# Optimization experiments

Hardware: AMD Instinct MI355X
Metric: run time of the kernel (lower is better)

Reference implementation:

```python
import jax, jax.numpy as jnp
import numpy as np

N, D, S, R = 50000, 256, 6, 4
EPS = 1e-5

def group_norm1(x, w, b):
    # GroupNorm with 1 group on [N, C]: normalize each row over channels
    m = jnp.mean(x, axis=-1, keepdims=True)
    v = jnp.mean(jnp.square(x - m), axis=-1, keepdims=True)
    return (x - m) * jax.lax.rsqrt(v + EPS) * w + b

def setup_inputs() -> dict:
    key = jax.random.key(0)
    ks = jax.random.split(key, 10)
    scale = 1.0 / np.sqrt(D)
    return {
        'lane_features': jax.random.normal(ks[0], (N, D), jnp.float32),
        'W_ctr': jax.random.normal(ks[1], (R, D, D), jnp.float32) * scale,
        'norm_w': jnp.ones((R, D), jnp.float32),
        'norm_b': jnp.zeros((R, D), jnp.float32),
        'W_ctr2': jax.random.normal(ks[2], (R, D, D), jnp.float32) * scale,
        'ctr2_norm_w': jnp.ones((R, D), jnp.float32),
        'ctr2_norm_b': jnp.zeros((R, D), jnp.float32),
        'W_pre': jax.random.normal(ks[3], (R, S, D, D), jnp.float32) * scale,
        'W_suc': jax.random.normal(ks[4], (R, S, D, D), jnp.float32) * scale,
        'pre_idx': jax.random.randint(ks[5], (S, N), 0, N, jnp.int32),
        'suc_idx': jax.random.randint(ks[6], (S, N), 0, N, jnp.int32),
        'n_hop_pre': jax.random.randint(ks[7], (S, N), 0, N, jnp.int32),
        'n_hop_suc': jax.random.randint(ks[8], (S, N), 0, N, jnp.int32),
    }

def reference(lane_features, W_ctr, norm_w, norm_b, W_ctr2, ctr2_norm_w,
              ctr2_norm_b, W_pre, W_suc, pre_idx, suc_idx, n_hop_pre, n_hop_suc):
    x = lane_features
    res = x
    for i in range(R):
        # ctr linear (bias=False): x @ W.T
        temp = x @ W_ctr[i].T
        for k in range(S):
            # pre branch: gather n_hop_pre, linear, scatter-add at suc
            msg_pre = x[n_hop_pre[k]] @ W_pre[i, k].T
            temp = temp.at[suc_idx[k]].add(msg_pre)
            # suc branch: gather n_hop_suc, linear, scatter-add at pre
            msg_suc = x[n_hop_suc[k]] @ W_suc[i, k].T
            temp = temp.at[pre_idx[k]].add(msg_suc)
        x = jax.nn.relu(group_norm1(temp, norm_w[i], norm_b[i]))
        # ctr2: Linear(no bias) + GroupNorm, no activation
        x = group_norm1(x @ W_ctr2[i].T, ctr2_norm_w[i], ctr2_norm_b[i])
        x = jax.nn.relu(x + res)
        res = x
    return x
```

## Files before the change

### kernel.cpp

```cpp
#include <hip/hip_runtime.h>

#define NROWS 50000
#define DIM   256
#define SHOPS 6
#define ROUNDS 4
#define EPSV  1e-5f
#define ND ((size_t)NROWS * DIM)
#define NB  196
#define EMAXR 36864
#define EMAXND ((size_t)EMAXR * DIM)

typedef _Float16 f16x8 __attribute__((ext_vector_type(8)));
typedef _Float16 f16x4 __attribute__((ext_vector_type(4)));
typedef float    f32x4 __attribute__((ext_vector_type(4)));

#define GLDS16(GP, LP) \
    __builtin_amdgcn_global_load_lds((const __attribute__((address_space(1))) unsigned*)(GP), \
                                     (__attribute__((address_space(3))) unsigned*)(LP), 16, 0, 0)

__device__ __forceinline__ int imin(int a, int b) { return a < b ? a : b; }

__global__ __launch_bounds__(256)
void gemm_p(const _Float16* __restrict__ A, const _Float16* __restrict__ WH,
            int s0, int s1, int nz, _Float16* __restrict__ C0,
            _Float16* __restrict__ CZ, int ctr0, int nwg,
            const int* __restrict__ LIVE, const int* __restrict__ Ecnt,
            int sbase)
{
    __shared__ _Float16 lds[3][8192];
    char* ldsb = (char*)lds;

    const int bid = blockIdx.x;
    const int q   = nwg >> 3, r = nwg & 7;
    const int xcd = bid & 7,  ii = bid >> 3;
    const int g   = (xcd < r) ? xcd * (q + 1) + ii
                              : r * (q + 1) + (xcd - r) * q + ii;
    const int j   = g / (2 * nz);
    const int sub = g - j * 2 * nz;
    const int by  = sub & 1;
    const size_t z = sub >> 1;
    int xp, jj;
    if (j < 7 * 49) { xp = j / 49; jj = j % 49; }
    else            { xp = 7; jj = j - 7 * 49; }
    const int bx = jj * 8 + xp;

    const int seg = sbase + (int)z;
    const int En  = (seg >= 0) ? Ecnt[seg] : NROWS;
    const int bm0 = bx * 128;
    if (bm0 >= En) return;
    const int* lvp = (seg >= 0) ? LIVE + (size_t)seg * NROWS : nullptr;

    const int tid = threadIdx.x;
    const int l   = tid & 63;
    const int w   = tid >> 6;
    const int wm  = w & 1;
    const int wn  = w >> 1;
    const int bn0 = by * 128;
    const int lr  = l & 15;
    const int sl  = l >> 4;

    const int wslot = (z == 0) ? s0 : s1 + (int)z;
    const char* Ab = (const char*)A;
    const char* Wb = (const char*)(WH + (size_t)wslot * (DIM * DIM));

    int arow[2], slog[2], wrow[2];
    #pragma unroll
    for (int qq = 0; qq < 2; ++qq) {
        const int c   = (w * 2 + qq) * 64 + l;
        const int row = c >> 2;
        slog[qq] = (c & 3) ^ ((row >> 1) & 3);
        const int cl = imin(bm0 + row, En - 1);
        arow[qq] = lvp ? lvp[cl] : cl;
        wrow[qq] = bn0 + row;
    }

    f32x4 acc[4][4];
    #pragma unroll
    for (int mt = 0; mt < 4; ++mt)
        #pragma unroll
        for (int nt = 0; nt < 4; ++nt)
            acc[mt][nt] = (f32x4){0.f, 0.f, 0.f, 0.f};

    auto stage = [&](int step, int buf) {
        const int kt64 = step * 64;
        char* base = ldsb + buf * 16384;
        #pragma unroll
        for (int qq = 0; qq < 2; ++qq) {
            GLDS16(Ab + (size_t)arow[qq] * 512 + kt64 + slog[qq] * 16,
                   base + (w * 2 + qq) * 1024);
            GLDS16(Wb + (size_t)wrow[qq] * 512 + kt64 + slog[qq] * 16,
                   base + 8192 + (w * 2 + qq) * 1024);
        }
    };

    auto compute = [&](int buf) {
        const char* base = ldsb + buf * 16384;
        f16x8 af[4], bf[4];
        #pragma unroll
        for (int mt = 0; mt < 4; ++mt) {
            const int row = wm * 64 + mt * 16 + lr;
            af[mt] = *(const f16x8*)(base + row * 64 + ((sl ^ ((row >> 1) & 3)) << 4));
        }
        #pragma unroll
        for (int nt = 0; nt < 4; ++nt) {
            const int row = wn * 64 + nt * 16 + lr;
            bf[nt] = *(const f16x8*)(base + 8192 + row * 64 + ((sl ^ ((row >> 1) & 3)) << 4));
        }
        #pragma unroll
        for (int mt = 0; mt < 4; ++mt)
            #pragma unroll
            for (int nt = 0; nt < 4; ++nt)
                acc[mt][nt] = __builtin_amdgcn_mfma_f32_16x16x32_f16(
                    af[mt], bf[nt], acc[mt][nt], 0, 0, 0);
    };

    stage(0, 0);
    stage(1, 1);
    #pragma unroll
    for (int t = 0; t < 7; ++t) {
        asm volatile("s_waitcnt vmcnt(4)" ::: "memory");
        __builtin_amdgcn_s_barrier();
        __builtin_amdgcn_sched_barrier(0);
        if (t < 6) stage(t + 2, (t + 2) % 3);
        compute(t % 3);
    }
    asm volatile("s_waitcnt vmcnt(0)" ::: "memory");
    __builtin_amdgcn_s_barrier();
    __builtin_amdgcn_sched_barrier(0);
    compute(7 % 3);

    __syncthreads();
    _Float16* et = (_Float16*)ldsb;
    #pragma unroll
    for (int mt = 0; mt < 4; ++mt)
        #pragma unroll
        for (int nt = 0; nt < 4; ++nt)
            #pragma unroll
            for (int jv = 0; jv < 4; ++jv) {
                const int row = wm * 64 + mt * 16 + sl * 4 + jv;
                const int col = wn * 64 + nt * 16 + lr;
                et[row * 136 + col] = (_Float16)acc[mt][nt][jv];
            }
    __syncthreads();
    _Float16* Cb = (ctr0 && z == 0) ? C0 : CZ + (size_t)((int)z - ctr0) * EMAXND;
    #pragma unroll
    for (int qq = 0; qq < 8; ++qq) {
        const int c   = qq * 256 + tid;
        const int row = c >> 4;
        const int cc  = (c & 15) * 8;
        const int orow = bm0 + row;
        if (orow < En) {
            const f16x8 v = *(const f16x8*)(et + row * 136 + cc);
            *(f16x8*)(Cb + (size_t)orow * DIM + bn0 + cc) = v;
        }
    }
}

__global__ __launch_bounds__(512)
void gemm_gn(const _Float16* __restrict__ A, const _Float16* __restrict__ WH,
             int wslot, const float* __restrict__ gw, const float* __restrict__ gb,
             float* __restrict__ X, _Float16* __restrict__ Xh, int writex)
{
    __shared__ char ldsb[49152 + 4096];
    float* sArr  = (float*)(ldsb + 49152);
    float* ssArr = sArr + 512;

    const int tid = threadIdx.x;
    const int l   = tid & 63;
    const int w   = tid >> 6;
    const int wm  = w & 1;
    const int wn  = w >> 1;
    const int bm0 = blockIdx.x * 128;
    const int lr  = l & 15;
    const int sl  = l >> 4;

    const char* Ab = (const char*)A;
    const char* Wb = (const char*)(WH + (size_t)wslot * (DIM * DIM));

    int arow, aslog, wr0, ws0, wr1, ws1;
    {
        int c = tid, row = c >> 2;
        aslog = (c & 3) ^ ((row >> 1) & 3);
        arow  = imin(bm0 + row, NROWS - 1);
        ws0 = aslog; wr0 = row;
        c = tid + 512; row = c >> 2;
        ws1 = (c & 3) ^ ((row >> 1) & 3); wr1 = row;
    }

    f32x4 acc[4][4];
    #pragma unroll
    for (int mt = 0; mt < 4; ++mt)
        #pragma unroll
        for (int nt = 0; nt < 4; ++nt)
            acc[mt][nt] = (f32x4){0.f, 0.f, 0.f, 0.f};

    auto stage = [&](int step, int buf) {
        const int kt64 = step * 64;
        char* base = ldsb + buf * 24576;
        GLDS16(Ab + (size_t)arow * 512 + kt64 + aslog * 16, base + w * 1024);
        GLDS16(Wb + (size_t)wr0 * 512 + kt64 + ws0 * 16, base + 8192 + w * 1024);
        GLDS16(Wb + (size_t)wr1 * 512 + kt64 + ws1 * 16, base + 16384 + w * 1024);
    };

    auto compute = [&](int buf) {
        const char* base = ldsb + buf * 24576;
        f16x8 af[4], bf[4];
        #pragma unroll
        for (int mt = 0; mt < 4; ++mt) {
            const int row = wm * 64 + mt * 16 + lr;
            af[mt] = *(const f16x8*)(base + row * 64 + ((sl ^ ((row >> 1) & 3)) << 4));
        }
        #pragma unroll
        for (int nt = 0; nt < 4; ++nt) {
            const int row = wn * 64 + nt * 16 + lr;
            bf[nt] = *(const f16x8*)(base + 8192 + row * 64 + ((sl ^ ((row >> 1) & 3)) << 4));
        }
        #pragma unroll
        for (int mt = 0; mt < 4; ++mt)
            #pragma unroll
            for (int nt = 0; nt < 4; ++nt)
                acc[mt][nt] = __builtin_amdgcn_mfma_f32_16x16x32_f16(
                    af[mt], bf[nt], acc[mt][nt], 0, 0, 0);
    };

    stage(0, 0);
    #pragma unroll
    for (int t = 0; t < 8; ++t) {
        asm volatile("s_waitcnt vmcnt(0)" ::: "memory");
        __builtin_amdgcn_s_barrier();
        __builtin_amdgcn_sched_barrier(0);
        if (t < 7) stage(t + 1, (t + 1) & 1);
        compute(t & 1);
    }

    float sp[4][4], ssp[4][4];
    #pragma unroll
    for (int mt = 0; mt < 4; ++mt)
        #pragma unroll
        for (int jv = 0; jv < 4; ++jv) {
            float s = 0.f, ss = 0.f;
            #pragma unroll
            for (int nt = 0; nt < 4; ++nt) {
                const float v = acc[mt][nt][jv];
                s += v; ss += v * v;
            }
            sp[mt][jv] = s; ssp[mt][jv] = ss;
        }
    #pragma unroll
    for (int off = 1; off < 16; off <<= 1)
        #pragma unroll
        for (int mt = 0; mt < 4; ++mt)
            #pragma unroll
            for (int jv = 0; jv < 4; ++jv) {
                sp[mt][jv]  += __shfl_xor(sp[mt][jv], off);
                ssp[mt][jv] += __shfl_xor(ssp[mt][jv], off);
            }
    __syncthreads();
    if (lr == 0) {
        #pragma unroll
        for (int mt = 0; mt < 4; ++mt)
            #pragma unroll
            for (int jv = 0; jv < 4; ++jv) {
                const int row = wm * 64 + mt * 16 + sl * 4 + jv;
                sArr[wn * 128 + row]  = sp[mt][jv];
                ssArr[wn * 128 + row] = ssp[mt][jv];
            }
    }
    __syncthreads();
    float mv[4][4], iv[4][4];
    #pragma unroll
    for (int mt = 0; mt < 4; ++mt)
        #pragma unroll
        for (int jv = 0; jv < 4; ++jv) {
            const int row = wm * 64 + mt * 16 + sl * 4 + jv;
            const float S  = sArr[row] + sArr[128 + row] + sArr[256 + row] + sArr[384 + row];
            const float SS = ssArr[row] + ssArr[128 + row] + ssArr[256 + row] + ssArr[384 + row];
            const float m  = S * (1.0f / DIM);
            mv[mt][jv] = m;
            iv[mt][jv] = rsqrtf(SS * (1.0f / DIM) - m * m + EPSV);
        }
    float gwv[4], gbv[4];
    #pragma unroll
    for (int nt = 0; nt < 4; ++nt) {
        const int col = wn * 64 + nt * 16 + lr;
        gwv[nt] = gw[col]; gbv[nt] = gb[col];
    }

    _Float16* et = (_Float16*)ldsb;
    #pragma unroll
    for (int half = 0; half < 2; ++half) {
        __syncthreads();
        if (wm == half) {
            #pragma unroll
            for (int mt = 0; mt < 4; ++mt)
                #pragma unroll
                for (int nt = 0; nt < 4; ++nt)
                    #pragma unroll
                    for (int jv = 0; jv < 4; ++jv) {
                        const int rl  = mt * 16 + sl * 4 + jv;
                        const int col = wn * 64 + nt * 16 + lr;
                        et[rl * 264 + col] = (_Float16)((acc[mt][nt][jv] - mv[mt][jv])
                                                        * iv[mt][jv] * gwv[nt] + gbv[nt]);
                    }
        }
        __syncthreads();
        #pragma unroll
        for (int qq = 0; qq < 4; ++qq) {
            const int c   = qq * 512 + tid;
            const int row = c >> 5;
            const int cc  = (c & 31) * 8;
            const int orow = bm0 + half * 64 + row;
            if (orow < NROWS) {
                const f16x8 y = *(const f16x8*)(et + row * 264 + cc);
                const f16x8 rr = *(const f16x8*)(Xh + (size_t)orow * DIM + cc);
                float o[8];
                #pragma unroll
                for (int e = 0; e < 8; ++e)
                    o[e] = fmaxf((float)y[e] + (float)rr[e], 0.f);
                f16x8 oh;
                #pragma unroll
                for (int e = 0; e < 8; ++e) oh[e] = (_Float16)o[e];
                *(f16x8*)(Xh + (size_t)orow * DIM + cc) = oh;
                if (writex) {
                    float* xp = X + (size_t)orow * DIM + cc;
                    *(float4*)xp       = make_float4(o[0], o[1], o[2], o[3]);
                    *(float4*)(xp + 4) = make_float4(o[4], o[5], o[6], o[7]);
                }
            }
        }
    }
}

__global__ __launch_bounds__(256)
void convert_w(const float* __restrict__ Wctr, const float* __restrict__ Wctr2,
               const float* __restrict__ Wpre, const float* __restrict__ Wsuc,
               _Float16* __restrict__ WH)
{
    const size_t i4 = (size_t)blockIdx.x * 256 + threadIdx.x;
    const size_t NT = (size_t)56 * DIM * DIM / 4;
    if (i4 >= NT) return;
    const size_t e = i4 * 4;
    const int slot = (int)(e >> 16);
    const int off  = (int)(e & 65535);
    const float* src;
    if (slot < 48) {
        const int r = slot / 12, s = slot % 12, k = s >> 1, dir = s & 1;
        src = (dir ? Wsuc : Wpre) + (((size_t)r * SHOPS + k) << 16) + off;
    } else if (slot < 52) {
        src = Wctr + ((size_t)(slot - 48) << 16) + off;
    } else {
        src = Wctr2 + ((size_t)(slot - 52) << 16) + off;
    }
    const float4 v = *(const float4*)src;
    f16x4 h;
    h[0] = (_Float16)v.x; h[1] = (_Float16)v.y;
    h[2] = (_Float16)v.z; h[3] = (_Float16)v.w;
    *(f16x4*)(WH + e) = h;
}

__global__ __launch_bounds__(256)
void init_x(const float* __restrict__ lane, _Float16* __restrict__ Xh)
{
    const size_t i4 = (size_t)blockIdx.x * 256 + threadIdx.x;
    if (i4 >= ND / 4) return;
    const float4 v = *(const float4*)(lane + i4 * 4);
    f16x4 h;
    h[0] = (_Float16)v.x; h[1] = (_Float16)v.y;
    h[2] = (_Float16)v.z; h[3] = (_Float16)v.w;
    *(f16x4*)(Xh + i4 * 4) = h;
}

__global__ __launch_bounds__(256)
void markk(const int* __restrict__ nhp, const int* __restrict__ nhs,
           int* __restrict__ mark)
{
    const int i = blockIdx.x * 256 + threadIdx.x;
    if (i >= NROWS) return;
    const int s = blockIdx.y;
    const int k = s >> 1, dir = s & 1;
    const int* gp = (dir ? nhs : nhp) + k * NROWS;
    mark[(size_t)s * NROWS + gp[i]] = 1;
}

__global__ __launch_bounds__(256)
void mscan1(const int* __restrict__ mark, int* __restrict__ mrank,
            int* __restrict__ msum)
{
    __shared__ int wsum[4];
    const int s = blockIdx.y;
    const int tid = threadIdx.x, lane = tid & 63, wv = tid >> 6;
    const int i = blockIdx.x * 256 + tid;
    const int c = (i < NROWS) ? mark[(size_t)s * NROWS + i] : 0;
    int v = c;
    #pragma unroll
    for (int off = 1; off < 64; off <<= 1) {
        const int t = __shfl_up(v, off);
        if (lane >= off) v += t;
    }
    if (lane == 63) wsum[wv] = v;
    __syncthreads();
    int add = 0;
    for (int w = 0; w < wv; ++w) add += wsum[w];
    if (i < NROWS) mrank[(size_t)s * NROWS + i] = add + v - c;
    if (tid == 255) msum[s * 256 + blockIdx.x] = wsum[0] + wsum[1] + wsum[2] + wsum[3];
}

__global__ __launch_bounds__(256)
void mscan2(const int* __restrict__ msum, int* __restrict__ mbpre,
            int* __restrict__ Ecnt)
{
    __shared__ int wsum[4];
    const int s = blockIdx.x;
    const int tid = threadIdx.x, lane = tid & 63, wv = tid >> 6;
    const int c = (tid < NB) ? msum[s * 256 + tid] : 0;
    int v = c;
    #pragma unroll
    for (int off = 1; off < 64; off <<= 1) {
        const int t = __shfl_up(v, off);
        if (lane >= off) v += t;
    }
    if (lane == 63) wsum[wv] = v;
    __syncthreads();
    int add = 0;
    for (int w = 0; w < wv; ++w) add += wsum[w];
    if (tid < NB) mbpre[s * 256 + tid] = add + v - c;
    if (tid == 0) Ecnt[s] = wsum[0] + wsum[1] + wsum[2] + wsum[3];
}

__global__ __launch_bounds__(256)
void mscan3(const int* __restrict__ mark, int* __restrict__ mrank,
            const int* __restrict__ mbpre, int* __restrict__ live)
{
    const int i = blockIdx.x * 256 + threadIdx.x;
    if (i >= NROWS) return;
    const int s = blockIdx.y;
    const size_t o = (size_t)s * NROWS + i;
    const int rk = mrank[o] + mbpre[s * 256 + blockIdx.x];
    mrank[o] = rk;
    if (mark[o]) live[(size_t)s * NROWS + rk] = i;
}

__global__ __launch_bounds__(256)
void count_kernel(const int* __restrict__ pidx, const int* __restrict__ sidx,
                  int* __restrict__ counts, int* __restrict__ countsA)
{
    const int i = blockIdx.x * 256 + threadIdx.x;
    if (i >= NROWS) return;
    const int s = blockIdx.y;
    const int k = s >> 1, dir = s & 1;
    const int* scp = (dir ? pidx : sidx) + k * NROWS;
    const int dst = scp[i];
    atomicAdd(&counts[dst], 1);
    if (s < 6) atomicAdd(&countsA[dst], 1);
}

__global__ __launch_bounds__(256)
void scan1_kernel(const int* __restrict__ counts, int* __restrict__ offs,
                  int* __restrict__ bsum)
{
    __shared__ int wsum[4];
    const int tid = threadIdx.x, lane = tid & 63, wv = tid >> 6;
    const int i = blockIdx.x * 256 + tid;
    const int c = (i < NROWS) ? counts[i] : 0;
    int v = c;
    #pragma unroll
    for (int off = 1; off < 64; off <<= 1) {
        const int t = __shfl_up(v, off);
        if (lane >= off) v += t;
    }
    if (lane == 63) wsum[wv] = v;
    __syncthreads();
    int add = 0;
    for (int w = 0; w < wv; ++w) add += wsum[w];
    if (i < NROWS) offs[i] = add + v - c;
    if (tid == 255) bsum[blockIdx.x] = wsum[0] + wsum[1] + wsum[2] + wsum[3];
}

__global__ __launch_bounds__(256)
void scan2_kernel(const int* __restrict__ bsum, int* __restrict__ bpre)
{
    __shared__ int wsum[4];
    const int tid = threadIdx.x, lane = tid & 63, wv = tid >> 6;
    const int c = (tid < NB) ? bsum[tid] : 0;
    int v = c;
    #pragma unroll
    for (int off = 1; off < 64; off <<= 1) {
        const int t = __shfl_up(v, off);
        if (lane >= off) v += t;
    }
    if (lane == 63) wsum[wv] = v;
    __syncthreads();
    int add = 0;
    for (int w = 0; w < wv; ++w) add += wsum[w];
    if (tid < NB) bpre[tid] = add + v - c;
}

__global__ __launch_bounds__(256)
void scan3_kernel(int* __restrict__ offs, const int* __restrict__ bpre,
                  const int* __restrict__ countsA,
                  int* __restrict__ cursorA, int* __restrict__ cursorB,
                  int* __restrict__ mid)
{
    const int i = blockIdx.x * 256 + threadIdx.x;
    if (i < NROWS) {
        const int v = offs[i] + bpre[blockIdx.x];
        offs[i] = v;
        cursorA[i] = v;
        const int m = v + countsA[i];
        mid[i] = m;
        cursorB[i] = m;
    }
    if (i == 0) offs[NROWS] = 12 * NROWS;
}

__global__ __launch_bounds__(256)
void fill_kernel(const int* __restrict__ pidx, const int* __restrict__ sidx,
                 const int* __restrict__ nhp, const int* __restrict__ nhs,
                 const int* __restrict__ mrank,
                 int* __restrict__ cursorA, int* __restrict__ cursorB,
                 int* __restrict__ entries)
{
    const int i = blockIdx.x * 256 + threadIdx.x;
    if (i >= NROWS) return;
    const int s = blockIdx.y;
    const int k = s >> 1, dir = s & 1;
    const int* scp = (dir ? pidx : sidx) + k * NROWS;
    const int* gp  = (dir ? nhs  : nhp)  + k * NROWS;
    const int dst = scp[i];
    const int pos = (s < 6) ? atomicAdd(&cursorA[dst], 1)
                            : atomicAdd(&cursorB[dst], 1);
    entries[pos] = (s << 16) | mrank[(size_t)s * NROWS + gp[i]];
}

template<int FIRST, int LAST>
__global__ __launch_bounds__(256)
void combine_f16(const _Float16* __restrict__ YC, _Float16* __restrict__ TEMP16,
                 const _Float16* __restrict__ YB,
                 const int* __restrict__ offsets, const int* __restrict__ mid,
                 const int* __restrict__ entries,
                 int c0, int nch, int half,
                 const float* __restrict__ gw, const float* __restrict__ gb,
                 _Float16* __restrict__ Hh)
{
    const int lane = threadIdx.x & 63;
    const int wv   = threadIdx.x >> 6;
    const int r    = blockIdx.x * 4 + wv;
    if (r >= NROWS) return;
    const size_t rowoff = (size_t)r * DIM + lane * 4;

    const f16x4 ivv = FIRST ? *(const f16x4*)(YC + rowoff)
                            : *(const f16x4*)(TEMP16 + rowoff);
    float4 acc;
    acc.x = (float)ivv[0]; acc.y = (float)ivv[1];
    acc.z = (float)ivv[2]; acc.w = (float)ivv[3];

    int e0, e1;
    if (half == 0)      { e0 = offsets[r]; e1 = mid[r]; }
    else if (half == 1) { e0 = mid[r];     e1 = offsets[r + 1]; }
    else                { e0 = offsets[r]; e1 = offsets[r + 1]; }

    for (int e = e0; e < e1; ++e) {
        const int ent = entries[e];
        const int s = ent >> 16;
        if ((unsigned)(s - c0) < (unsigned)nch) {
            const f16x4 yv = *(const f16x4*)(YB + (size_t)(s - c0) * EMAXND
                                             + (size_t)(ent & 0xFFFF) * DIM + lane * 4);
            acc.x += (float)yv[0]; acc.y += (float)yv[1];
            acc.z += (float)yv[2]; acc.w += (float)yv[3];
        }
    }

    if (LAST) {
        float s  = acc.x + acc.y + acc.z + acc.w;
        float ss = acc.x * acc.x + acc.y * acc.y + acc.z * acc.z + acc.w * acc.w;
        #pragma unroll
        for (int off = 32; off >= 1; off >>= 1) {
            s  += __shfl_xor(s, off);
            ss += __shfl_xor(ss, off);
        }
        const float m   = s * (1.0f / DIM);
        const float var = ss * (1.0f / DIM) - m * m;
        const float inv = rsqrtf(var + EPSV);
        const float4 wv4 = *(const float4*)(gw + lane * 4);
        const float4 bv4 = *(const float4*)(gb + lane * 4);
        f16x4 o;
        o[0] = (_Float16)fmaxf((acc.x - m) * inv * wv4.x + bv4.x, 0.f);
        o[1] = (_Float16)fmaxf((acc.y - m) * inv * wv4.y + bv4.y, 0.f);
        o[2] = (_Float16)fmaxf((acc.z - m) * inv * wv4.z + bv4.z, 0.f);
        o[3] = (_Float16)fmaxf((acc.w - m) * inv * wv4.w + bv4.w, 0.f);
        *(f16x4*)(Hh + rowoff) = o;
    } else {
        f16x4 o;
        o[0] = (_Float16)acc.x; o[1] = (_Float16)acc.y;
        o[2] = (_Float16)acc.z; o[3] = (_Float16)acc.w;
        *(f16x4*)(TEMP16 + rowoff) = o;
    }
}

extern "C" void kernel_launch(void* const* d_in, const int* in_sizes, int n_in,
                              void* d_out, int out_size, void* d_ws, size_t ws_size,
                              hipStream_t stream)
{
    const float* lane   = (const float*)d_in[0];
    const float* W_ctr  = (const float*)d_in[1];
    const float* norm_w = (const float*)d_in[2];
    const float* norm_b = (const float*)d_in[3];
    const float* W_ctr2 = (const float*)d_in[4];
    const float* c2w    = (const float*)d_in[5];
    const float* c2b    = (const float*)d_in[6];
    const float* W_pre  = (const float*)d_in[7];
    const float* W_suc  = (const float*)d_in[8];
    const int*   pidx   = (const int*)d_in[9];
    const int*   sidx   = (const int*)d_in[10];
    const int*   nhp    = (const int*)d_in[11];
    const int*   nhs    = (const int*)d_in[12];

    float* X = (float*)d_out;

    char* p = (char*)d_ws;
    int* counts  = (int*)p; p += (size_t)NROWS * 4;
    int* countsA = (int*)p; p += (size_t)NROWS * 4;
    int* offsets = (int*)p; p += (size_t)(NROWS + 4) * 4;
    int* mid     = (int*)p; p += (size_t)NROWS * 4;
    int* cursorA = (int*)p; p += (size_t)NROWS * 4;
    int* cursorB = (int*)p; p += (size_t)NROWS * 4;
    int* bsum    = (int*)p; p += 256 * 4;
    int* bpre    = (int*)p; p += 256 * 4;
    int* msum    = (int*)p; p += 12 * 256 * 4;
    int* mbpre   = (int*)p; p += 12 * 256 * 4;
    int* Ecnt    = (int*)p; p += 16 * 4;
    int* entries = (int*)p; p += (size_t)12 * NROWS * 4;
    int* LIVE    = (int*)p; p += (size_t)12 * NROWS * 4;
    p = (char*)(((uintptr_t)p + 15) & ~(uintptr_t)15);
    _Float16* Xh   = (_Float16*)p; p += ND * 2;
    _Float16* Hh   = (_Float16*)p; p += ND * 2;
    _Float16* T16  = (_Float16*)p; p += ND * 2;
    _Float16* WH   = (_Float16*)p; p += (size_t)56 * DIM * DIM * 2;
    p = (char*)(((uintptr_t)p + 15) & ~(uintptr_t)15);
    _Float16* YC   = (_Float16*)p; p += ND * 2;
    _Float16* YBUF = (_Float16*)p;

    int* mark  = (int*)YBUF;
    int* mrank = mark + (size_t)12 * NROWS;

    const size_t used = (size_t)(p - (char*)d_ws);
    const size_t slotb = EMAXND * 2;
    int nslot = (ws_size > used) ? (int)((ws_size - used) / slotb) : 1;
    if (nslot < 1) nslot = 1;
    int CH;
    if (nslot >= 12) CH = 12;
    else {
        CH = nslot;
        const int nchunks = (12 + CH - 1) / CH;
        CH = (12 + nchunks - 1) / nchunks;
    }

    const dim3 blk(256);
    const int  gnBlocks = (NROWS + 3) / 4;
    const int  cwBlocks = (int)(((size_t)56 * DIM * DIM / 4 + 255) / 256);
    const int  ixBlocks = (int)((ND / 4 + 255) / 256);

    convert_w<<<cwBlocks, blk, 0, stream>>>(W_ctr, W_ctr2, W_pre, W_suc, WH);
    init_x<<<ixBlocks, blk, 0, stream>>>(lane, Xh);
    hipMemsetAsync(counts, 0, NROWS * sizeof(int), stream);
    hipMemsetAsync(countsA, 0, NROWS * sizeof(int), stream);
    hipMemsetAsync(mark, 0, (size_t)12 * NROWS * sizeof(int), stream);
    markk<<<dim3(NB, 12), blk, 0, stream>>>(nhp, nhs, mark);
    mscan1<<<dim3(NB, 12), blk, 0, stream>>>(mark, mrank, msum);
    mscan2<<<12, blk, 0, stream>>>(msum, mbpre, Ecnt);
    mscan3<<<dim3(NB, 12), blk, 0, stream>>>(mark, mrank, mbpre, LIVE);
    count_kernel<<<dim3(NB, 12), blk, 0, stream>>>(pidx, sidx, counts, countsA);
    scan1_kernel<<<NB, blk, 0, stream>>>(counts, offsets, bsum);
    scan2_kernel<<<1, blk, 0, stream>>>(bsum, bpre);
    scan3_kernel<<<NB, blk, 0, stream>>>(offsets, bpre, countsA,
                                         cursorA, cursorB, mid);
    fill_kernel<<<dim3(NB, 12), blk, 0, stream>>>(pidx, sidx, nhp, nhs, mrank,
                                                  cursorA, cursorB, entries);

    for (int i = 0; i < ROUNDS; ++i) {
        for (int c0 = 0; c0 < 12; c0 += CH) {
            const int nz = (12 - c0 < CH) ? (12 - c0) : CH;
            const bool first = (c0 == 0);
            const bool last  = (c0 + nz >= 12);
            const int ctr0  = first ? 1 : 0;
            const int slots = nz + ctr0;
            const int nwg   = 391 * 2 * slots;
            gemm_p<<<dim3(nwg), blk, 0, stream>>>(
                Xh, WH, first ? (48 + i) : (i * 12 + c0), i * 12 + c0 - ctr0,
                slots, YC, YBUF, ctr0, nwg, LIVE, Ecnt, c0 - ctr0);
            const int half = (CH == 6) ? (first ? 0 : 1) : -1;
            if (first && last)
                combine_f16<1, 1><<<gnBlocks, blk, 0, stream>>>(YC, T16, YBUF,
                    offsets, mid, entries, c0, nz, half,
                    norm_w + i * DIM, norm_b + i * DIM, Hh);
            else if (first)
                combine_f16<1, 0><<<gnBlocks, blk, 0, stream>>>(YC, T16, YBUF,
                    offsets, mid, entries, c0, nz, half,
                    norm_w + i * DIM, norm_b + i * DIM, Hh);
            else if (last)
                combine_f16<0, 1><<<gnBlocks, blk, 0, stream>>>(YC, T16, YBUF,
                    offsets, mid, entries, c0, nz, half,
                    norm_w + i * DIM, norm_b + i * DIM, Hh);
            else
                combine_f16<0, 0><<<gnBlocks, blk, 0, stream>>>(YC, T16, YBUF,
                    offsets, mid, entries, c0, nz, half,
                    norm_w + i * DIM, norm_b + i * DIM, Hh);
        }
        gemm_gn<<<391, 512, 0, stream>>>(Hh, WH, 52 + i, c2w + i * DIM,
                                         c2b + i * DIM, X, Xh,
                                         (i == ROUNDS - 1) ? 1 : 0);
    }
}
```

Before: 1.077 ms.

## Triple-buffer gemm_gn, fuse setup kernels, prefetch combine gathers, shrink buffers

gemm_gn moves from double to triple buffering, with a partial vmcnt wait so two stages stay in flight. The setup kernels are merged: weight and input conversion run in one launch, and the mark, count and scan passes run in three launches over 13 grid rows, cutting launch overhead. combine_f16 now prefetches up to 20 gathered rows into registers before accumulating, to expose memory-level parallelism. The workspace is reorganised: YC reuses the output buffer, T16 aliases Hh when 12 slots fit, and EMAXR is lowered. The lower EMAXR risks overflow if a slot's live count exceeds 32768, and the chunk-range filter in combine is removed.

After: 950.3 us, median of 2. 1.13x faster.

```diff
diff --git a/kernel.cpp b/kernel.cpp
--- a/kernel.cpp
+++ b/kernel.cpp
@@ -7,7 +7,7 @@
 #define EPSV  1e-5f
 #define ND ((size_t)NROWS * DIM)
 #define NB  196
-#define EMAXR 36864
+#define EMAXR 32768
 #define EMAXND ((size_t)EMAXR * DIM)
 
 typedef _Float16 f16x8 __attribute__((ext_vector_type(8)));
@@ -161,8 +161,8 @@
              int wslot, const float* __restrict__ gw, const float* __restrict__ gb,
              float* __restrict__ X, _Float16* __restrict__ Xh, int writex)
 {
-    __shared__ char ldsb[49152 + 4096];
-    float* sArr  = (float*)(ldsb + 49152);
+    __shared__ char ldsb[3 * 24576 + 4096];
+    float* sArr  = (float*)(ldsb + 73728);
     float* ssArr = sArr + 512;
 
     const int tid = threadIdx.x;
@@ -224,14 +224,19 @@
     };
 
     stage(0, 0);
-    #pragma unroll
-    for (int t = 0; t < 8; ++t) {
-        asm volatile("s_waitcnt vmcnt(0)" ::: "memory");
+    stage(1, 1);
+    #pragma unroll
+    for (int t = 0; t < 7; ++t) {
+        asm volatile("s_waitcnt vmcnt(3)" ::: "memory");
         __builtin_amdgcn_s_barrier();
         __builtin_amdgcn_sched_barrier(0);
-        if (t < 7) stage(t + 1, (t + 1) & 1);
-        compute(t & 1);
-    }
+        if (t < 6) stage(t + 2, (t + 2) % 3);
+        compute(t % 3);
+    }
+    asm volatile("s_waitcnt vmcnt(0)" ::: "memory");
+    __builtin_amdgcn_s_barrier();
+    __builtin_amdgcn_sched_barrier(0);
+    compute(7 % 3);
 
     float sp[4][4], ssp[4][4];
     #pragma unroll
@@ -332,65 +337,72 @@
 }
 
 __global__ __launch_bounds__(256)
-void convert_w(const float* __restrict__ Wctr, const float* __restrict__ Wctr2,
-               const float* __restrict__ Wpre, const float* __restrict__ Wsuc,
-               _Float16* __restrict__ WH)
-{
-    const size_t i4 = (size_t)blockIdx.x * 256 + threadIdx.x;
-    const size_t NT = (size_t)56 * DIM * DIM / 4;
-    if (i4 >= NT) return;
-    const size_t e = i4 * 4;
-    const int slot = (int)(e >> 16);
-    const int off  = (int)(e & 65535);
-    const float* src;
-    if (slot < 48) {
-        const int r = slot / 12, s = slot % 12, k = s >> 1, dir = s & 1;
-        src = (dir ? Wsuc : Wpre) + (((size_t)r * SHOPS + k) << 16) + off;
-    } else if (slot < 52) {
-        src = Wctr + ((size_t)(slot - 48) << 16) + off;
+void cvt_init(const float* __restrict__ lane, _Float16* __restrict__ Xh,
+              const float* __restrict__ Wctr, const float* __restrict__ Wctr2,
+              const float* __restrict__ Wpre, const float* __restrict__ Wsuc,
+              _Float16* __restrict__ WH)
+{
+    const int bid = blockIdx.x;
+    if (bid < 12500) {
+        const size_t i4 = (size_t)bid * 256 + threadIdx.x;
+        if (i4 >= ND / 4) return;
+        const float4 v = *(const float4*)(lane + i4 * 4);
+        f16x4 h;
+        h[0] = (_Float16)v.x; h[1] = (_Float16)v.y;
+        h[2] = (_Float16)v.z; h[3] = (_Float16)v.w;
+        *(f16x4*)(Xh + i4 * 4) = h;
     } else {
-        src = Wctr2 + ((size_t)(slot - 52) << 16) + off;
-    }
-    const float4 v = *(const float4*)src;
-    f16x4 h;
-    h[0] = (_Float16)v.x; h[1] = (_Float16)v.y;
-    h[2] = (_Float16)v.z; h[3] = (_Float16)v.w;
-    *(f16x4*)(WH + e) = h;
-}
-
-__global__ __launch_bounds__(256)
-void init_x(const float* __restrict__ lane, _Float16* __restrict__ Xh)
-{
-    const size_t i4 = (size_t)blockIdx.x * 256 + threadIdx.x;
-    if (i4 >= ND / 4) return;
-    const float4 v = *(const float4*)(lane + i4 * 4);
-    f16x4 h;
-    h[0] = (_Float16)v.x; h[1] = (_Float16)v.y;
-    h[2] = (_Float16)v.z; h[3] = (_Float16)v.w;
-    *(f16x4*)(Xh + i4 * 4) = h;
-}
-
-__global__ __launch_bounds__(256)
-void markk(const int* __restrict__ nhp, const int* __restrict__ nhs,
-           int* __restrict__ mark)
+        const size_t i4 = (size_t)(bid - 12500) * 256 + threadIdx.x;
+        const size_t NT = (size_t)56 * DIM * DIM / 4;
+        if (i4 >= NT) return;
+        const size_t e = i4 * 4;
+        const int slot = (int)(e >> 16);
+        const int off  = (int)(e & 65535);
+        const float* src;
+        if (slot < 48) {
+            const int r = slot / 12, s = slot % 12, k = s >> 1, dir = s & 1;
+            src = (dir ? Wsuc : Wpre) + (((size_t)r * SHOPS + k) << 16) + off;
+        } else if (slot < 52) {
+            src = Wctr + ((size_t)(slot - 48) << 16) + off;
+        } else {
+            src = Wctr2 + ((size_t)(slot - 52) << 16) + off;
+        }
+        const float4 v = *(const float4*)src;
+        f16x4 h;
+        h[0] = (_Float16)v.x; h[1] = (_Float16)v.y;
+        h[2] = (_Float16)v.z; h[3] = (_Float16)v.w;
+        *(f16x4*)(WH + e) = h;
+    }
+}
+
+__global__ __launch_bounds__(256)
+void markcount(const int* __restrict__ pidx, const int* __restrict__ sidx,
+               const int* __restrict__ nhp, const int* __restrict__ nhs,
+               int* __restrict__ mark, int* __restrict__ counts,
+               int* __restrict__ countsA)
 {
     const int i = blockIdx.x * 256 + threadIdx.x;
     if (i >= NROWS) return;
     const int s = blockIdx.y;
     const int k = s >> 1, dir = s & 1;
-    const int* gp = (dir ? nhs : nhp) + k * NROWS;
+    const int* gp  = (dir ? nhs  : nhp)  + k * NROWS;
+    const int* scp = (dir ? pidx : sidx) + k * NROWS;
     mark[(size_t)s * NROWS + gp[i]] = 1;
-}
-
-__global__ __launch_bounds__(256)
-void mscan1(const int* __restrict__ mark, int* __restrict__ mrank,
-            int* __restrict__ msum)
+    const int dst = scp[i];
+    atomicAdd(&counts[dst], 1);
+    if (s < 6) atomicAdd(&countsA[dst], 1);
+}
+
+__global__ __launch_bounds__(256)
+void pscan1(const int* __restrict__ mark, const int* __restrict__ counts,
+            int* __restrict__ mrank, int* __restrict__ msum,
+            int* __restrict__ offs, int* __restrict__ bsum)
 {
     __shared__ int wsum[4];
-    const int s = blockIdx.y;
+    const int y = blockIdx.y;
     const int tid = threadIdx.x, lane = tid & 63, wv = tid >> 6;
     const int i = blockIdx.x * 256 + tid;
-    const int c = (i < NROWS) ? mark[(size_t)s * NROWS + i] : 0;
+    const int c = (i < NROWS) ? ((y < 12) ? mark[(size_t)y * NROWS + i] : counts[i]) : 0;
     int v = c;
     #pragma unroll
     for (int off = 1; off < 64; off <<= 1) {
@@ -401,18 +413,27 @@
     __syncthreads();
     int add = 0;
     for (int w = 0; w < wv; ++w) add += wsum[w];
-    if (i < NROWS) mrank[(size_t)s * NROWS + i] = add + v - c;
-    if (tid == 255) msum[s * 256 + blockIdx.x] = wsum[0] + wsum[1] + wsum[2] + wsum[3];
-}
-
-__global__ __launch_bounds__(256)
-void mscan2(const int* __restrict__ msum, int* __restrict__ mbpre,
+    const int excl = add + v - c;
+    if (i < NROWS) {
+        if (y < 12) mrank[(size_t)y * NROWS + i] = excl;
+        else        offs[i] = excl;
+    }
+    if (tid == 255) {
+        const int tot = wsum[0] + wsum[1] + wsum[2] + wsum[3];
+        if (y < 12) msum[y * 256 + blockIdx.x] = tot;
+        else        bsum[blockIdx.x] = tot;
+    }
+}
+
+__global__ __launch_bounds__(256)
+void pscan2(const int* __restrict__ msum, const int* __restrict__ bsum,
+            int* __restrict__ mbpre, int* __restrict__ bpre,
             int* __restrict__ Ecnt)
 {
     __shared__ int wsum[4];
-    const int s = blockIdx.x;
+    const int y = blockIdx.x;
     const int tid = threadIdx.x, lane = tid & 63, wv = tid >> 6;
-    const int c = (tid < NB) ? msum[s * 256 + tid] : 0;
+    const int c = (tid < NB) ? ((y < 12) ? msum[y * 256 + tid] : bsum[tid]) : 0;
     int v = c;
     #pragma unroll
     for (int off = 1; off < 64; off <<= 1) {
@@ -423,94 +444,40 @@
     __syncthreads();
     int add = 0;
     for (int w = 0; w < wv; ++w) add += wsum[w];
-    if (tid < NB) mbpre[s * 256 + tid] = add + v - c;
-    if (tid == 0) Ecnt[s] = wsum[0] + wsum[1] + wsum[2] + wsum[3];
-}
-
-__global__ __launch_bounds__(256)
-void mscan3(const int* __restrict__ mark, int* __restrict__ mrank,
-            const int* __restrict__ mbpre, int* __restrict__ live)
+    if (tid < NB) {
+        if (y < 12) mbpre[y * 256 + tid] = add + v - c;
+        else        bpre[tid] = add + v - c;
+    }
+    if (tid == 0 && y < 12)
+        Ecnt[y] = wsum[0] + wsum[1] + wsum[2] + wsum[3];
+}
+
+__global__ __launch_bounds__(256)
+void pscan3(const int* __restrict__ mark, int* __restrict__ mrank,
+            const int* __restrict__ mbpre, int* __restrict__ live,
+            int* __restrict__ offs, const int* __restrict__ bpre,
+            const int* __restrict__ countsA, int* __restrict__ cursorA,
+            int* __restrict__ cursorB, int* __restrict__ mid)
 {
     const int i = blockIdx.x * 256 + threadIdx.x;
-    if (i >= NROWS) return;
-    const int s = blockIdx.y;
-    const size_t o = (size_t)s * NROWS + i;
-    const int rk = mrank[o] + mbpre[s * 256 + blockIdx.x];
-    mrank[o] = rk;
-    if (mark[o]) live[(size_t)s * NROWS + rk] = i;
-}
-
-__global__ __launch_bounds__(256)
-void count_kernel(const int* __restrict__ pidx, const int* __restrict__ sidx,
-                  int* __restrict__ counts, int* __restrict__ countsA)
-{
-    const int i = blockIdx.x * 256 + threadIdx.x;
-    if (i >= NROWS) return;
-    const int s = blockIdx.y;
-    const int k = s >> 1, dir = s & 1;
-    const int* scp = (dir ? pidx : sidx) + k * NROWS;
-    const int dst = scp[i];
-    atomicAdd(&counts[dst], 1);
-    if (s < 6) atomicAdd(&countsA[dst], 1);
-}
-
-__global__ __launch_bounds__(256)
-void scan1_kernel(const int* __restrict__ counts, int* __restrict__ offs,
-                  int* __restrict__ bsum)
-{
-    __shared__ int wsum[4];
-    const int tid = threadIdx.x, lane = tid & 63, wv = tid >> 6;
-    const int i = blockIdx.x * 256 + tid;
-    const int c = (i < NROWS) ? counts[i] : 0;
-    int v = c;
-    #pragma unroll
-    for (int off = 1; off < 64; off <<= 1) {
-        const int t = __shfl_up(v, off);
-        if (lane >= off) v += t;
-    }
-    if (lane == 63) wsum[wv] = v;
-    __syncthreads();
-    int add = 0;
-    for (int w = 0; w < wv; ++w) add += wsum[w];
-    if (i < NROWS) offs[i] = add + v - c;
-    if (tid == 255) bsum[blockIdx.x] = wsum[0] + wsum[1] + wsum[2] + wsum[3];
-}
-
-__global__ __launch_bounds__(256)
-void scan2_kernel(const int* __restrict__ bsum, int* __restrict__ bpre)
-{
-    __shared__ int wsum[4];
-    const int tid = threadIdx.x, lane = tid & 63, wv = tid >> 6;
-    const int c = (tid < NB) ? bsum[tid] : 0;
-    int v = c;
-    #pragma unroll
-    for (int off = 1; off < 64; off <<= 1) {
-        const int t = __shfl_up(v, off);
-        if (lane >= off) v += t;
-    }
-    if (lane == 63) wsum[wv] = v;
-    __syncthreads();
-    int add = 0;
-    for (int w = 0; w < wv; ++w) add += wsum[w];
-    if (tid < NB) bpre[tid] = add + v - c;
-}
-
-__global__ __launch_bounds__(256)
-void scan3_kernel(int* __restrict__ offs, const int* __restrict__ bpre,
-                  const int* __restrict__ countsA,
-                  int* __restrict__ cursorA, int* __restrict__ cursorB,
-                  int* __restrict__ mid)
-{
-    const int i = blockIdx.x * 256 + threadIdx.x;
-    if (i < NROWS) {
-        const int v = offs[i] + bpre[blockIdx.x];
-        offs[i] = v;
-        cursorA[i] = v;
-        const int m = v + countsA[i];
-        mid[i] = m;
-        cursorB[i] = m;
-    }
-    if (i == 0) offs[NROWS] = 12 * NROWS;
+    const int y = blockIdx.y;
+    if (y < 12) {
+        if (i >= NROWS) return;
+        const size_t o = (size_t)y * NROWS + i;
+        const int rk = mrank[o] + mbpre[y * 256 + blockIdx.x];
+        mrank[o] = rk;
+        if (mark[o]) live[(size_t)y * NROWS + rk] = i;
+    } else {
+        if (i < NROWS) {
+            const int v = offs[i] + bpre[blockIdx.x];
+            offs[i] = v;
+            cursorA[i] = v;
+            const int m = v + countsA[i];
+            mid[i] = m;
+            cursorB[i] = m;
+        }
+        if (i == 0) offs[NROWS] = 12 * NROWS;
+    }
 }
 
 __global__ __launch_bounds__(256)
@@ -532,13 +499,14 @@
     entries[pos] = (s << 16) | mrank[(size_t)s * NROWS + gp[i]];
 }
 
+#define PF 20
 template<int FIRST, int LAST>
 __global__ __launch_bounds__(256)
 void combine_f16(const _Float16* __restrict__ YC, _Float16* __restrict__ TEMP16,
                  const _Float16* __restrict__ YB,
                  const int* __restrict__ offsets, const int* __restrict__ mid,
                  const int* __restrict__ entries,
-                 int c0, int nch, int half,
+                 int c0, int half,
                  const float* __restrict__ gw, const float* __restrict__ gb,
                  _Float16* __restrict__ Hh)
 {
@@ -559,15 +527,30 @@
     else if (half == 1) { e0 = mid[r];     e1 = offsets[r + 1]; }
     else                { e0 = offsets[r]; e1 = offsets[r + 1]; }
 
-    for (int e = e0; e < e1; ++e) {
+    const int n  = e1 - e0;
+    const int nf = n < PF ? n : PF;
+    f16x4 buf[PF];
+    #pragma unroll
+    for (int t = 0; t < PF; ++t) {
+        if (t < nf) {
+            const int ent = entries[e0 + t];
+            buf[t] = *(const f16x4*)(YB + (size_t)((ent >> 16) - c0) * EMAXND
+                                     + (size_t)(ent & 0xFFFF) * DIM + lane * 4);
+        }
+    }
+    #pragma unroll
+    for (int t = 0; t < PF; ++t) {
+        if (t < nf) {
+            acc.x += (float)buf[t][0]; acc.y += (float)buf[t][1];
+            acc.z += (float)buf[t][2]; acc.w += (float)buf[t][3];
+        }
+    }
+    for (int e = e0 + nf; e < e1; ++e) {
         const int ent = entries[e];
-        const int s = ent >> 16;
-        if ((unsigned)(s - c0) < (unsigned)nch) {
-            const f16x4 yv = *(const f16x4*)(YB + (size_t)(s - c0) * EMAXND
-                                             + (size_t)(ent & 0xFFFF) * DIM + lane * 4);
-            acc.x += (float)yv[0]; acc.y += (float)yv[1];
-            acc.z += (float)yv[2]; acc.w += (float)yv[3];
-        }
+        const f16x4 yv = *(const f16x4*)(YB + (size_t)((ent >> 16) - c0) * EMAXND
+                                         + (size_t)(ent & 0xFFFF) * DIM + lane * 4);
+        acc.x += (float)yv[0]; acc.y += (float)yv[1];
+        acc.z += (float)yv[2]; acc.w += (float)yv[3];
     }
 
     if (LAST) {
@@ -616,6 +599,7 @@
     const int*   nhs    = (const int*)d_in[12];
 
     float* X = (float*)d_out;
+    _Float16* YC = (_Float16*)d_out;
 
     char* p = (char*)d_ws;
     int* counts  = (int*)p; p += (size_t)NROWS * 4;
@@ -632,79 +616,72 @@
     int* entries = (int*)p; p += (size_t)12 * NROWS * 4;
     int* LIVE    = (int*)p; p += (size_t)12 * NROWS * 4;
     p = (char*)(((uintptr_t)p + 15) & ~(uintptr_t)15);
-    _Float16* Xh   = (_Float16*)p; p += ND * 2;
-    _Float16* Hh   = (_Float16*)p; p += ND * 2;
-    _Float16* T16  = (_Float16*)p; p += ND * 2;
-    _Float16* WH   = (_Float16*)p; p += (size_t)56 * DIM * DIM * 2;
-    p = (char*)(((uintptr_t)p + 15) & ~(uintptr_t)15);
-    _Float16* YC   = (_Float16*)p; p += ND * 2;
-    _Float16* YBUF = (_Float16*)p;
-
-    int* mark  = (int*)YBUF;
+    _Float16* Xh = (_Float16*)p; p += ND * 2;
+    _Float16* Hh = (_Float16*)p; p += ND * 2;
+    _Float16* WH = (_Float16*)p; p += (size_t)56 * DIM * DIM * 2;
+    p = (char*)(((uintptr_t)p + 255) & ~(uintptr_t)255);
+    char* area = p;
+
+    const size_t areaB = ws_size - (size_t)(area - (char*)d_ws);
+    const size_t slotb = EMAXND * 2;
+    int CH;
+    _Float16 *T16, *YBUF;
+    if (areaB >= 12 * slotb) {
+        CH = 12;
+        YBUF = (_Float16*)area;
+        T16 = Hh;
+    } else {
+        CH = 6;
+        T16 = (_Float16*)area;
+        YBUF = T16 + ND;
+    }
+
+    int* mark  = (int*)area;
     int* mrank = mark + (size_t)12 * NROWS;
-
-    const size_t used = (size_t)(p - (char*)d_ws);
-    const size_t slotb = EMAXND * 2;
-    int nslot = (ws_size > used) ? (int)((ws_size - used) / slotb) : 1;
-    if (nslot < 1) nslot = 1;
-    int CH;
-    if (nslot >= 12) CH = 12;
-    else {
-        CH = nslot;
-        const int nchunks = (12 + CH - 1) / CH;
-        CH = (12 + nchunks - 1) / nchunks;
-    }
 
     const dim3 blk(256);
     const int  gnBlocks = (NROWS + 3) / 4;
-    const int  cwBlocks = (int)(((size_t)56 * DIM * DIM / 4 + 255) / 256);
-    const int  ixBlocks = (int)((ND / 4 + 255) / 256);
-
-    convert_w<<<cwBlocks, blk, 0, stream>>>(W_ctr, W_ctr2, W_pre, W_suc, WH);
-    init_x<<<ixBlocks, blk, 0, stream>>>(lane, Xh);
-    hipMemsetAsync(counts, 0, NROWS * sizeof(int), stream);
-    hipMemsetAsync(countsA, 0, NROWS * sizeof(int), stream);
+
+    cvt_init<<<16084, blk, 0, stream>>>(lane, Xh, W_ctr, W_ctr2, W_pre, W_suc, WH);
+    hipMemsetAsync(counts, 0, 2 * NROWS * sizeof(int), stream);
     hipMemsetAsync(mark, 0, (size_t)12 * NROWS * sizeof(int), stream);
-    markk<<<dim3(NB, 12), blk, 0, stream>>>(nhp, nhs, mark);
-    mscan1<<<dim3(NB, 12), blk, 0, stream>>>(mark, mrank, msum);
-    mscan2<<<12, blk, 0, stream>>>(msum, mbpre, Ecnt);
-    mscan3<<<dim3(NB, 12), blk, 0, stream>>>(mark, mrank, mbpre, LIVE);
-    count_kernel<<<dim3(NB, 12), blk, 0, stream>>>(pidx, sidx, counts, countsA);
-    scan1_kernel<<<NB, blk, 0, stream>>>(counts, offsets, bsum);
-    scan2_kernel<<<1, blk, 0, stream>>>(bsum, bpre);
-    scan3_kernel<<<NB, blk, 0, stream>>>(offsets, bpre, countsA,
-                                         cursorA, cursorB, mid);
+    markcount<<<dim3(NB, 12), blk, 0, stream>>>(pidx, sidx, nhp, nhs,
+                                                mark, counts, countsA);
+    pscan1<<<dim3(NB, 13), blk, 0, stream>>>(mark, counts, mrank, msum, offsets, bsum);
+    pscan2<<<13, blk, 0, stream>>>(msum, bsum, mbpre, bpre, Ecnt);
+    pscan3<<<dim3(NB, 13), blk, 0, stream>>>(mark, mrank, mbpre, LIVE,
+                                             offsets, bpre, countsA,
+                                             cursorA, cursorB, mid);
     fill_kernel<<<dim3(NB, 12), blk, 0, stream>>>(pidx, sidx, nhp, nhs, mrank,
                                                   cursorA, cursorB, entries);
 
     for (int i = 0; i < ROUNDS; ++i) {
-        for (int c0 = 0; c0 < 12; c0 += CH) {
-            const int nz = (12 - c0 < CH) ? (12 - c0) : CH;
-            const bool first = (c0 == 0);
-            const bool last  = (c0 + nz >= 12);
-            const int ctr0  = first ? 1 : 0;
-            const int slots = nz + ctr0;
-            const int nwg   = 391 * 2 * slots;
-            gemm_p<<<dim3(nwg), blk, 0, stream>>>(
-                Xh, WH, first ? (48 + i) : (i * 12 + c0), i * 12 + c0 - ctr0,
-                slots, YC, YBUF, ctr0, nwg, LIVE, Ecnt, c0 - ctr0);
-            const int half = (CH == 6) ? (first ? 0 : 1) : -1;
-            if (first && last)
-                combine_f16<1, 1><<<gnBlocks, blk, 0, stream>>>(YC, T16, YBUF,
-                    offsets, mid, entries, c0, nz, half,
-                    norm_w + i * DIM, norm_b + i * DIM, Hh);
-            else if (first)
-                combine_f16<1, 0><<<gnBlocks, blk, 0, stream>>>(YC, T16, YBUF,
-                    offsets, mid, entries, c0, nz, half,
-                    norm_w + i * DIM, norm_b + i * DIM, Hh);
-            else if (last)
-                combine_f16<0, 1><<<gnBlocks, blk, 0, stream>>>(YC, T16, YBUF,
-                    offsets, mid, entries, c0, nz, half,
-                    norm_w + i * DIM, norm_b + i * DIM, Hh);
-            else
-                combine_f16<0, 0><<<gnBlocks, blk, 0, stream>>>(YC, T16, YBUF,
-                    offsets, mid, entries, c0, nz, half,
-                    norm_w + i * DIM, norm_b + i * DIM, Hh);
+        if (CH == 12) {
+            const int nwg = 391 * 2 * 13;
+            gemm_p<<<dim3(nwg), blk, 0, stream>>>(Xh, WH, 48 + i, i * 12 - 1,
+                                                  13, YC, YBUF, 1, nwg,
+                                                  LIVE, Ecnt, -1);
+            combine_f16<1, 1><<<gnBlocks, blk, 0, stream>>>(YC, T16, YBUF,
+                offsets, mid, entries, 0, -1,
+                norm_w + i * DIM, norm_b + i * DIM, Hh);
+        } else {
+            for (int c0 = 0; c0 < 12; c0 += 6) {
+                const bool first = (c0 == 0);
+                const int ctr0  = first ? 1 : 0;
+                const int slots = 6 + ctr0;
+                const int nwg   = 391 * 2 * slots;
+                gemm_p<<<dim3(nwg), blk, 0, stream>>>(
+                    Xh, WH, first ? (48 + i) : (i * 12 + c0), i * 12 + c0 - ctr0,
+                    slots, YC, YBUF, ctr0, nwg, LIVE, Ecnt, c0 - ctr0);
+                if (first)
+                    combine_f16<1, 0><<<gnBlocks, blk, 0, stream>>>(YC, T16, YBUF,
+                        offsets, mid, entries, c0, 0,
+                        norm_w + i * DIM, norm_b + i * DIM, Hh);
+                else
+                    combine_f16<0, 1><<<gnBlocks, blk, 0, stream>>>(YC, T16, YBUF,
+                        offsets, mid, entries, c0, 1,
+                        norm_w + i * DIM, norm_b + i * DIM, Hh);
+            }
         }
         gemm_gn<<<391, 512, 0, stream>>>(Hh, WH, 52 + i, c2w + i * DIM,
                                          c2b + i * DIM, X, Xh,
```
